# Kernel tuning notes

Measured on AMD Instinct MI355X. Metric: run time of the kernel, lower is better.

The kernel has to match this reference:

```python
import jax, jax.numpy as jnp
import numpy as np

D_MODEL = 1024
D_STATE = 16
D_CONV = 4
EXPAND = 2
D_INNER = EXPAND * D_MODEL  # 2048
DT_RANK = (D_MODEL + 15) // 16  # 64
BATCH = 2
SEQ = 1024


def setup_inputs() -> dict:
    key = jax.random.key(0)
    ks = jax.random.split(key, 9)
    s = 0.02
    x = jax.random.normal(ks[0], (BATCH, SEQ, D_MODEL), jnp.float32)
    W_in = jax.random.normal(ks[1], (D_MODEL, 2 * D_INNER), jnp.float32) * s
    conv_w = jax.random.normal(ks[2], (D_INNER, D_CONV), jnp.float32) * s
    conv_b = jnp.zeros((D_INNER,), jnp.float32)
    W_x = jax.random.normal(ks[3], (D_INNER, DT_RANK + 2 * D_STATE), jnp.float32) * s
    W_dt = jax.random.normal(ks[4], (DT_RANK, D_INNER), jnp.float32) * (DT_RANK ** -0.5)
    # dt bias init: inverse softplus of dt ~ U(1e-3, 0.1)
    dt0 = jax.random.uniform(ks[5], (D_INNER,), jnp.float32, 1e-3, 0.1)
    b_dt = dt0 + jnp.log(-jnp.expm1(-dt0))
    # S4D-real A init: A[d, n] = -(n+1)
    A_log = jnp.log(jnp.tile(jnp.arange(1, D_STATE + 1, dtype=jnp.float32), (D_INNER, 1)))
    D_skip = jnp.ones((D_INNER,), jnp.float32)
    W_out = jax.random.normal(ks[6], (D_INNER, D_MODEL), jnp.float32) * s
    return {"x": x, "W_in": W_in, "conv_w": conv_w, "conv_b": conv_b,
            "W_x": W_x, "W_dt": W_dt, "b_dt": b_dt, "A_log": A_log,
            "D_skip": D_skip, "W_out": W_out}


def _mamba_forward(x, W_in, conv_w, conv_b, W_x, W_dt, b_dt, A_log, D_skip, W_out):
    Bsz, L, _ = x.shape
    # input projection -> [B, L, 2*d_inner], split into stream and gate
    xz = x @ W_in
    xr, z = jnp.split(xz, 2, axis=-1)
    # depthwise causal conv1d over time
    xt = xr.transpose(0, 2, 1)                       # [B, d_inner, L]
    kern = conv_w[:, None, :]                        # [d_inner, 1, d_conv]
    xc = jax.lax.conv_general_dilated(
        xt, kern, window_strides=(1,), padding=[(D_CONV - 1, 0)],
        feature_group_count=D_INNER, dimension_numbers=("NCH", "OIH", "NCH"))
    xc = jax.nn.silu(xc + conv_b[None, :, None]).transpose(0, 2, 1)  # [B, L, d_inner]
    # data-dependent dt, B, C
    dbl = xc @ W_x                                   # [B, L, dt_rank + 2*d_state]
    dt, Bm, Cm = jnp.split(dbl, [DT_RANK, DT_RANK + D_STATE], axis=-1)
    dt = jax.nn.softplus(dt @ W_dt + b_dt)           # [B, L, d_inner]
    A = -jnp.exp(A_log)                              # [d_inner, d_state]

    def step(h, inp):
        dt_t, B_t, C_t, x_t = inp                    # [B,d_inner],[B,d_state],[B,d_state],[B,d_inner]
        dA = jnp.exp(dt_t[..., None] * A)            # [B, d_inner, d_state]
        h = dA * h + (dt_t * x_t)[..., None] * B_t[:, None, :]
        y = jnp.einsum("bds,bs->bd", h, C_t)
        return h, y

    h0 = jnp.zeros((Bsz, D_INNER, D_STATE), x.dtype)
    xs = (dt.transpose(1, 0, 2), Bm.transpose(1, 0, 2),
          Cm.transpose(1, 0, 2), xc.transpose(1, 0, 2))
    _, ys = jax.lax.scan(step, h0, xs)               # ys: [L, B, d_inner]
    y = ys.transpose(1, 0, 2) + xc * D_skip
    y = y * jax.nn.silu(z)
    return y @ W_out                                 # [B, L, d_model]


def reference(x, W_in, conv_w, conv_b, W_x, W_dt, b_dt, A_log, D_skip, W_out):
    return _mamba_forward(x, W_in, conv_w, conv_b, W_x, W_dt, b_dt, A_log, D_skip, W_out)
```

## Files before the change

kernel.cpp:

```cpp
#include <hip/hip_runtime.h>

#define BATCH 2
#define SEQL 1024
#define DMODEL 1024
#define DINNER 2048
#define DSTATE 16
#define DTRANK 64
#define NCH 64
#define LC 16

typedef short bf16x8 __attribute__((ext_vector_type(8)));
typedef float f32x4 __attribute__((ext_vector_type(4)));
typedef int i32x4 __attribute__((ext_vector_type(4)));

__device__ __forceinline__ unsigned short f2bf(float f) {
  unsigned u = __float_as_uint(f);
  return (unsigned short)((u + 0x7fffu + ((u >> 16) & 1u)) >> 16);
}
__device__ __forceinline__ float bf2f(unsigned short u) {
  return __uint_as_float((unsigned)u << 16);
}
__device__ __forceinline__ float sigmoidf_(float x) { return 1.f / (1.f + __expf(-x)); }

__device__ __forceinline__ void gl_lds16(const unsigned short* g, unsigned short* l) {
  __builtin_amdgcn_global_load_lds(
      (const __attribute__((address_space(1))) unsigned int*)g,
      (__attribute__((address_space(3))) unsigned int*)l, 16, 0, 0);
}

#define BM 128
#define BN 128

__global__ __launch_bounds__(256) void k_gemm_mfma(
    const unsigned short* __restrict__ A,
    const unsigned short* __restrict__ Bt,
    float* __restrict__ C, unsigned short* __restrict__ C2,
    int M, int N, int K, const float* __restrict__ bias, int mode)
{
  __shared__ __attribute__((aligned(16))) unsigned short As[128 * 64];
  __shared__ __attribute__((aligned(16))) unsigned short Bs[128 * 64];
  const int tid = threadIdx.x;
  const int wave = tid >> 6, lane = tid & 63;
  const int gx = gridDim.x;
  const int nwg = gx * gridDim.y;
  const int flat = blockIdx.x + gx * blockIdx.y;
  const int sw = (flat & 7) * (nwg >> 3) + (flat >> 3);
  const int m0 = (sw % gx) * BM, n0 = (sw / gx) * BN;
  const int Kc = K / gridDim.z;
  const int k0beg = blockIdx.z * Kc;
  float* Cz = C + (size_t)blockIdx.z * M * N;
  unsigned short* C2z = C2 + (size_t)blockIdx.z * M * N;
  const int wr = (wave >> 1) * 64, wc = (wave & 1) * 64;
  const int fr = lane & 15;
  const int qw = lane >> 4;

  int srow[4], scol[4];
  #pragma unroll
  for (int i = 0; i < 4; ++i) {
    int off = wave * 4096 + i * 1024 + lane * 16;
    int row = off >> 7;
    int c16 = ((off >> 4) & 7) ^ (row & 7);
    srow[i] = row;
    scol[i] = c16 * 8;
  }

  f32x4 acc[4][4] = {};
  for (int k0 = k0beg; k0 < k0beg + Kc; k0 += 64) {
    #pragma unroll
    for (int i = 0; i < 4; ++i)
      gl_lds16(A + (size_t)(m0 + srow[i]) * K + k0 + scol[i],
               &As[(wave * 4096 + i * 1024) >> 1]);
    #pragma unroll
    for (int i = 0; i < 4; ++i)
      gl_lds16(Bt + (size_t)(n0 + srow[i]) * K + k0 + scol[i],
               &Bs[(wave * 4096 + i * 1024) >> 1]);
    __syncthreads();
    #pragma unroll
    for (int t = 0; t < 2; ++t) {
      bf16x8 af[4], bfv[4];
      #pragma unroll
      for (int i = 0; i < 4; ++i) {
        int row = wr + i * 16 + fr;
        int c16 = (t * 4 + qw) ^ (row & 7);
        af[i] = *(const bf16x8*)&As[row * 64 + c16 * 8];
      }
      #pragma unroll
      for (int j = 0; j < 4; ++j) {
        int row = wc + j * 16 + fr;
        int c16 = (t * 4 + qw) ^ (row & 7);
        bfv[j] = *(const bf16x8*)&Bs[row * 64 + c16 * 8];
      }
      #pragma unroll
      for (int i = 0; i < 4; ++i)
        #pragma unroll
        for (int j = 0; j < 4; ++j)
          acc[i][j] = __builtin_amdgcn_mfma_f32_16x16x32_bf16(af[i], bfv[j], acc[i][j], 0, 0, 0);
    }
    __syncthreads();
  }
  const int rr = qw * 4;
  if (mode == 1) {
    #pragma unroll
    for (int j = 0; j < 4; ++j) {
      float bj = bias[n0 + wc + j * 16 + fr];
      #pragma unroll
      for (int i = 0; i < 4; ++i)
        #pragma unroll
        for (int r = 0; r < 4; ++r) {
          float v = acc[i][j][r] + bj;
          C2[(size_t)(m0 + wr + i * 16 + rr + r) * N + (n0 + wc + j * 16 + fr)] =
              f2bf(__logf(1.f + __expf(v)));
        }
    }
  } else if (mode == 3) {
    #pragma unroll
    for (int i = 0; i < 4; ++i)
      #pragma unroll
      for (int j = 0; j < 4; ++j)
        #pragma unroll
        for (int r = 0; r < 4; ++r)
          C2z[(size_t)(m0 + wr + i * 16 + rr + r) * N + (n0 + wc + j * 16 + fr)] =
              f2bf(acc[i][j][r]);
  } else {
    #pragma unroll
    for (int i = 0; i < 4; ++i)
      #pragma unroll
      for (int j = 0; j < 4; ++j)
        #pragma unroll
        for (int r = 0; r < 4; ++r)
          Cz[(size_t)(m0 + wr + i * 16 + rr + r) * N + (n0 + wc + j * 16 + fr)] = acc[i][j][r];
  }
}

__global__ __launch_bounds__(256) void k_gemm_n64(
    const unsigned short* __restrict__ A,
    const unsigned short* __restrict__ Bt,
    unsigned short* __restrict__ C2, int M, int N, int K)
{
  __shared__ __attribute__((aligned(16))) unsigned short As[128 * 64];
  __shared__ __attribute__((aligned(16))) unsigned short Bs[64 * 64];
  const int tid = threadIdx.x;
  const int wave = tid >> 6, lane = tid & 63;
  const int gx = gridDim.x;
  const int nwg = gx * gridDim.y;
  const int flat = blockIdx.x + gx * blockIdx.y;
  const int sw = (flat & 7) * (nwg >> 3) + (flat >> 3);
  const int m0 = (sw % gx) * 128, n0 = (sw / gx) * 64;
  const int wr = (wave & 1) * 64, wc = (wave >> 1) * 32;
  const int fr = lane & 15;
  const int qw = lane >> 4;

  int srowA[4], scolA[4];
  #pragma unroll
  for (int i = 0; i < 4; ++i) {
    int off = wave * 4096 + i * 1024 + lane * 16;
    int row = off >> 7;
    int c16 = ((off >> 4) & 7) ^ (row & 7);
    srowA[i] = row;
    scolA[i] = c16 * 8;
  }
  int srowB[2], scolB[2];
  #pragma unroll
  for (int i = 0; i < 2; ++i) {
    int off = wave * 2048 + i * 1024 + lane * 16;
    int row = off >> 7;
    int c16 = ((off >> 4) & 7) ^ (row & 7);
    srowB[i] = row;
    scolB[i] = c16 * 8;
  }

  f32x4 acc[4][2] = {};
  for (int k0 = 0; k0 < K; k0 += 64) {
    #pragma unroll
    for (int i = 0; i < 4; ++i)
      gl_lds16(A + (size_t)(m0 + srowA[i]) * K + k0 + scolA[i],
               &As[(wave * 4096 + i * 1024) >> 1]);
    #pragma unroll
    for (int i = 0; i < 2; ++i)
      gl_lds16(Bt + (size_t)(n0 + srowB[i]) * K + k0 + scolB[i],
               &Bs[(wave * 2048 + i * 1024) >> 1]);
    __syncthreads();
    #pragma unroll
    for (int t = 0; t < 2; ++t) {
      bf16x8 af[4], bfv[2];
      #pragma unroll
      for (int i = 0; i < 4; ++i) {
        int row = wr + i * 16 + fr;
        int c16 = (t * 4 + qw) ^ (row & 7);
        af[i] = *(const bf16x8*)&As[row * 64 + c16 * 8];
      }
      #pragma unroll
      for (int j = 0; j < 2; ++j) {
        int row = wc + j * 16 + fr;
        int c16 = (t * 4 + qw) ^ (row & 7);
        bfv[j] = *(const bf16x8*)&Bs[row * 64 + c16 * 8];
      }
      #pragma unroll
      for (int i = 0; i < 4; ++i)
        #pragma unroll
        for (int j = 0; j < 2; ++j)
          acc[i][j] = __builtin_amdgcn_mfma_f32_16x16x32_bf16(af[i], bfv[j], acc[i][j], 0, 0, 0);
    }
    __syncthreads();
  }
  const int rr = qw * 4;
  #pragma unroll
  for (int i = 0; i < 4; ++i)
    #pragma unroll
    for (int j = 0; j < 2; ++j)
      #pragma unroll
      for (int r = 0; r < 4; ++r)
        C2[(size_t)(m0 + wr + i * 16 + rr + r) * N + (n0 + wc + j * 16 + fr)] =
            f2bf(acc[i][j][r]);
}

__device__ __forceinline__ void transpose_tile(
    const float* __restrict__ src, unsigned short* __restrict__ dst,
    int R, int C, int bx, int by, float* t )
{
  int bc = bx * 64, br = by * 64;
  int tr = threadIdx.x >> 2;
  int tc = (threadIdx.x & 3) * 16;
  #pragma unroll
  for (int i = 0; i < 4; ++i) {
    float4 v = *(const float4*)(src + (size_t)(br + tr) * C + bc + tc + i * 4);
    t[tr * 65 + tc + i * 4 + 0] = v.x; t[tr * 65 + tc + i * 4 + 1] = v.y;
    t[tr * 65 + tc + i * 4 + 2] = v.z; t[tr * 65 + tc + i * 4 + 3] = v.w;
  }
  __syncthreads();
  unsigned short tmp[16];
  #pragma unroll
  for (int i = 0; i < 16; ++i) tmp[i] = f2bf(t[(tc + i) * 65 + tr]);
  unsigned short* dp = dst + (size_t)(bc + tr) * R + br + tc;
  *(i32x4*)dp = *(i32x4*)&tmp[0];
  *(i32x4*)(dp + 8) = *(i32x4*)&tmp[8];
}

__global__ __launch_bounds__(256) void k_prep(
    const float* __restrict__ x,   unsigned short* __restrict__ xbf,
    const float* __restrict__ Win, unsigned short* __restrict__ wint,
    const float* __restrict__ Wout,unsigned short* __restrict__ woutt,
    const float* __restrict__ Wdt, unsigned short* __restrict__ wdtt,
    const float* __restrict__ Wx,  unsigned short* __restrict__ wxt)
{
  __shared__ float t[64 * 65];
  int bid = blockIdx.x;
  if (bid < 1024) {
    int i = (bid * 256 + threadIdx.x) * 8;
    float4 a = *(const float4*)(x + i);
    float4 b = *(const float4*)(x + i + 4);
    unsigned short tmp[8] = {f2bf(a.x), f2bf(a.y), f2bf(a.z), f2bf(a.w),
                             f2bf(b.x), f2bf(b.y), f2bf(b.z), f2bf(b.w)};
    *(i32x4*)(xbf + i) = *(i32x4*)tmp;
  } else if (bid < 2048) {
    int tt = bid - 1024;
    transpose_tile(Win, wint, 1024, 4096, tt & 63, tt >> 6, t);
  } else if (bid < 2560) {
    int tt = bid - 2048;
    transpose_tile(Wout, woutt, 2048, 1024, tt & 15, tt >> 4, t);
  } else if (bid < 2592) {
    int tt = bid - 2560;
    transpose_tile(Wdt, wdtt, 64, 2048, tt, 0, t);
  } else {
    int idx = (bid - 2592) * 256 + threadIdx.x;
    int k = idx & (DINNER - 1);
    int n = idx >> 11;
    float v = (n < 96) ? Wx[(size_t)k * 96 + n] : 0.f;
    wxt[idx] = f2bf(v);
  }
}

__global__ __launch_bounds__(256) void k_conv_silu(
    const unsigned short* __restrict__ xzb, const float* __restrict__ cw,
    const float* __restrict__ cb, unsigned short* __restrict__ xcb)
{
  int t = blockIdx.x * 256 + threadIdx.x;
  int idx = t * 8;
  int d0 = idx & (DINNER - 1);
  int bl = idx >> 11;
  int l = bl & (SEQL - 1);
  float s[8];
  {
    float4 c0 = *(const float4*)(cb + d0);
    float4 c1 = *(const float4*)(cb + d0 + 4);
    s[0] = c0.x; s[1] = c0.y; s[2] = c0.z; s[3] = c0.w;
    s[4] = c1.x; s[5] = c1.y; s[6] = c1.z; s[7] = c1.w;
  }
  float4 w[8];
  #pragma unroll
  for (int i = 0; i < 8; ++i) w[i] = *(const float4*)(cw + (d0 + i) * 4);
  #pragma unroll
  for (int k = 0; k < 4; ++k) {
    int ll = l - 3 + k;
    if (ll >= 0) {
      bf16x8 v = *(const bf16x8*)&xzb[(size_t)(bl - 3 + k) * 4096 + d0];
      #pragma unroll
      for (int i = 0; i < 8; ++i)
        s[i] += bf2f((unsigned short)v[i]) * ((const float*)&w[i])[k];
    }
  }
  unsigned short o[8];
  #pragma unroll
  for (int i = 0; i < 8; ++i) {
    float r = s[i] * sigmoidf_(s[i]);
    o[i] = f2bf(r);
  }
  *(i32x4*)&xcb[idx] = *(i32x4*)o;
}

__global__ void k_reduce2(const float* __restrict__ part, float* __restrict__ dbl,
                          unsigned short* __restrict__ dtraw)
{
  int idx = blockIdx.x * 256 + threadIdx.x;
  float s = 0.f;
  #pragma unroll
  for (int z = 0; z < 16; ++z) s += part[(size_t)z * 2048 * 128 + idx];
  dbl[idx] = s;
  int col = idx & 127, rw = idx >> 7;
  if (col < 64) dtraw[rw * 64 + col] = f2bf(s);
}

__global__ void k_reduce5(const unsigned short* __restrict__ part, float* __restrict__ out)
{
  int idx = (blockIdx.x * 256 + threadIdx.x) * 8;
  float s[8] = {};
  #pragma unroll
  for (int z = 0; z < 4; ++z) {
    bf16x8 v = *(const bf16x8*)(part + (size_t)z * 2048 * 1024 + idx);
    #pragma unroll
    for (int i = 0; i < 8; ++i) s[i] += bf2f((unsigned short)v[i]);
  }
  *(f32x4*)(out + idx) = *(f32x4*)&s[0];
  *(f32x4*)(out + idx + 4) = *(f32x4*)&s[4];
}

__global__ __launch_bounds__(256) void k_scan_A(
    const unsigned short* __restrict__ dtb, const unsigned short* __restrict__ xcb,
    const float* __restrict__ dbl, const float* __restrict__ Alog,
    float* __restrict__ hend, float* __restrict__ sumdtb)
{
  __shared__ __attribute__((aligned(16))) float bcB[LC][DSTATE];
  int gid = blockIdx.x * 256 + threadIdx.x;
  int d = gid & (DINNER - 1);
  int t = gid >> 11;
  int c = t & (NCH - 1);
  int b = t >> 6;
  const int r0 = b * SEQL + c * LC;
  bcB[threadIdx.x >> 4][threadIdx.x & 15] =
      dbl[(size_t)(r0 + (threadIdx.x >> 4)) * 128 + 64 + (threadIdx.x & 15)];
  float As[DSTATE];
  #pragma unroll
  for (int i = 0; i < 4; ++i) {
    f32x4 a = *(const f32x4*)&Alog[d * DSTATE + i * 4];
    #pragma unroll
    for (int j = 0; j < 4; ++j) As[i * 4 + j] = -__expf(a[j]);
  }
  __syncthreads();
  float h[DSTATE];
  #pragma unroll
  for (int s = 0; s < DSTATE; ++s) h[s] = 0.f;
  float sumdt = 0.f;
  #pragma unroll
  for (int li = 0; li < LC; li += 2) {
    float dt0 = bf2f(dtb[(size_t)(r0 + li) * DINNER + d]);
    float xv0 = bf2f(xcb[(size_t)(r0 + li) * DINNER + d]);
    float dt1 = bf2f(dtb[(size_t)(r0 + li + 1) * DINNER + d]);
    float xv1 = bf2f(xcb[(size_t)(r0 + li + 1) * DINNER + d]);
    f32x4 B0[4], B1[4];
    #pragma unroll
    for (int i = 0; i < 4; ++i) B0[i] = *(const f32x4*)&bcB[li][i * 4];
    #pragma unroll
    for (int i = 0; i < 4; ++i) B1[i] = *(const f32x4*)&bcB[li + 1][i * 4];
    float dtx0 = dt0 * xv0, dtx1 = dt1 * xv1;
    sumdt += dt0 + dt1;
    const float* Bv0 = (const float*)B0;
    const float* Bv1 = (const float*)B1;
    #pragma unroll
    for (int s = 0; s < DSTATE; ++s) {
      float dA0 = __expf(dt0 * As[s]);
      h[s] = dA0 * h[s] + dtx0 * Bv0[s];
      float dA1 = __expf(dt1 * As[s]);
      h[s] = dA1 * h[s] + dtx1 * Bv1[s];
    }
  }
  size_t base = ((size_t)(b * NCH + c) * DSTATE) * DINNER + d;
  #pragma unroll
  for (int s = 0; s < DSTATE; ++s) hend[base + (size_t)s * DINNER] = h[s];
  sumdtb[(size_t)(b * NCH + c) * DINNER + d] = sumdt;
}

__global__ void k_scan_B(const float* __restrict__ hend, const float* __restrict__ sumdtb,
                         const float* __restrict__ Alog, float* __restrict__ hin)
{
  int gid = blockIdx.x * 256 + threadIdx.x;
  int d = gid & (DINNER - 1);
  int s = (gid >> 11) & (DSTATE - 1);
  int b = gid >> 15;
  const float As = -__expf(Alog[d * DSTATE + s]);
  float h = 0.f;
  for (int c0 = 0; c0 < NCH; c0 += 8) {
    float he[8], sd[8];
    #pragma unroll
    for (int i = 0; i < 8; ++i) {
      he[i] = hend[((size_t)(b * NCH + c0 + i) * DSTATE + s) * DINNER + d];
      sd[i] = sumdtb[(size_t)(b * NCH + c0 + i) * DINNER + d];
    }
    #pragma unroll
    for (int i = 0; i < 8; ++i) {
      hin[((size_t)(b * NCH + c0 + i) * DSTATE + s) * DINNER + d] = h;
      h = __expf(sd[i] * As) * h + he[i];
    }
  }
}

__global__ __launch_bounds__(256) void k_scan_C(
    const unsigned short* __restrict__ dtb, const unsigned short* __restrict__ xcb,
    const float* __restrict__ dbl, const float* __restrict__ Alog,
    const float* __restrict__ hin, const float* __restrict__ Dskip,
    const unsigned short* __restrict__ xzb, unsigned short* __restrict__ yact)
{
  __shared__ __attribute__((aligned(16))) float bc[LC][32];
  int gid = blockIdx.x * 256 + threadIdx.x;
  int d = gid & (DINNER - 1);
  int t = gid >> 11;
  int c = t & (NCH - 1);
  int b = t >> 6;
  const int r0 = b * SEQL + c * LC;
  {
    int step = threadIdx.x >> 4, j = (threadIdx.x & 15) * 2;
    float2 v = *(const float2*)&dbl[(size_t)(r0 + step) * 128 + 64 + j];
    bc[step][j] = v.x; bc[step][j + 1] = v.y;
  }
  float As[DSTATE];
  #pragma unroll
  for (int i = 0; i < 4; ++i) {
    f32x4 a = *(const f32x4*)&Alog[d * DSTATE + i * 4];
    #pragma unroll
    for (int j = 0; j < 4; ++j) As[i * 4 + j] = -__expf(a[j]);
  }
  float h[DSTATE];
  size_t base = ((size_t)(b * NCH + c) * DSTATE) * DINNER + d;
  #pragma unroll
  for (int s = 0; s < DSTATE; ++s) h[s] = hin[base + (size_t)s * DINNER];
  const float dsk = Dskip[d];
  __syncthreads();
  #pragma unroll
  for (int li = 0; li < LC; li += 2) {
    const int r = r0 + li;
    float dt0 = bf2f(dtb[(size_t)r * DINNER + d]);
    float xv0 = bf2f(xcb[(size_t)r * DINNER + d]);
    float zv0 = bf2f(xzb[(size_t)r * 4096 + 2048 + d]);
    float dt1 = bf2f(dtb[(size_t)(r + 1) * DINNER + d]);
    float xv1 = bf2f(xcb[(size_t)(r + 1) * DINNER + d]);
    float zv1 = bf2f(xzb[(size_t)(r + 1) * 4096 + 2048 + d]);
    f32x4 B0[4], C0[4], B1[4], C1[4];
    #pragma unroll
    for (int i = 0; i < 4; ++i) B0[i] = *(const f32x4*)&bc[li][i * 4];
    #pragma unroll
    for (int i = 0; i < 4; ++i) C0[i] = *(const f32x4*)&bc[li][16 + i * 4];
    #pragma unroll
    for (int i = 0; i < 4; ++i) B1[i] = *(const f32x4*)&bc[li + 1][i * 4];
    #pragma unroll
    for (int i = 0; i < 4; ++i) C1[i] = *(const f32x4*)&bc[li + 1][16 + i * 4];
    const float* Bv0 = (const float*)B0; const float* Cv0 = (const float*)C0;
    const float* Bv1 = (const float*)B1; const float* Cv1 = (const float*)C1;
    float dtx0 = dt0 * xv0, dtx1 = dt1 * xv1;
    float y0 = 0.f, y1 = 0.f;
    #pragma unroll
    for (int s = 0; s < DSTATE; ++s) {
      float dA0 = __expf(dt0 * As[s]);
      h[s] = dA0 * h[s] + dtx0 * Bv0[s];
      y0 += h[s] * Cv0[s];
      float dA1 = __expf(dt1 * As[s]);
      h[s] = dA1 * h[s] + dtx1 * Bv1[s];
      y1 += h[s] * Cv1[s];
    }
    y0 += xv0 * dsk;
    y1 += xv1 * dsk;
    float ya0 = y0 * (zv0 * sigmoidf_(zv0));
    float ya1 = y1 * (zv1 * sigmoidf_(zv1));
    yact[(size_t)r * DINNER + d] = f2bf(ya0);
    yact[(size_t)(r + 1) * DINNER + d] = f2bf(ya1);
  }
}

extern "C" void kernel_launch(void* const* d_in, const int* in_sizes, int n_in,
                              void* d_out, int out_size, void* d_ws, size_t ws_size,
                              hipStream_t stream) {
  const float* x     = (const float*)d_in[0];
  const float* Win   = (const float*)d_in[1];
  const float* cw    = (const float*)d_in[2];
  const float* cbias = (const float*)d_in[3];
  const float* Wx    = (const float*)d_in[4];
  const float* Wdt   = (const float*)d_in[5];
  const float* bdt   = (const float*)d_in[6];
  const float* Alog  = (const float*)d_in[7];
  const float* Dsk   = (const float*)d_in[8];
  const float* Wout  = (const float*)d_in[9];
  float* out = (float*)d_out;

  char* ws = (char*)d_ws;
  const size_t MB = 1 << 20;
  unsigned short* xzb   = (unsigned short*)(ws);
  unsigned short* xbf   = (unsigned short*)(ws + 16 * MB);
  unsigned short* wint  = (unsigned short*)(ws + 20 * MB);
  unsigned short* xcb   = (unsigned short*)(ws + 28 * MB);
  unsigned short* wxt   = (unsigned short*)(ws + 36 * MB);
  float*          dbl   = (float*)         (ws + 37 * MB);
  unsigned short* dtraw = (unsigned short*)(ws + 38 * MB);
  unsigned short* wdtt  = (unsigned short*)(ws + 39 * MB);
  unsigned short* dtb16 = (unsigned short*)(ws + 40 * MB);
  float*          hend  = (float*)         (ws + 48 * MB);
  float*          sumdt = (float*)         (ws + 64 * MB);
  float*          hin   = (float*)         (ws + 66 * MB);
  unsigned short* yact  = (unsigned short*)(ws + 82 * MB);
  unsigned short* woutt = (unsigned short*)(ws + 90 * MB);
  float*          part2 = (float*)         (ws + 94 * MB);
  unsigned short* part5 = (unsigned short*)(ws + 110 * MB);
  (void)ws_size; (void)in_sizes; (void)n_in; (void)out_size;

  k_prep<<<3616, 256, 0, stream>>>(x, xbf, Win, wint, Wout, woutt, Wdt, wdtt, Wx, wxt);
  k_gemm_n64<<<dim3(16, 64), 256, 0, stream>>>(xbf, wint, xzb, 2048, 4096, 1024);
  k_conv_silu<<<2048, 256, 0, stream>>>(xzb, cw, cbias, xcb);
  k_gemm_mfma<<<dim3(16, 1, 16), 256, 0, stream>>>(xcb, wxt, part2, nullptr, 2048, 128, 2048, nullptr, 0);
  k_reduce2<<<1024, 256, 0, stream>>>(part2, dbl, dtraw);
  k_gemm_mfma<<<dim3(16, 16, 1), 256, 0, stream>>>(dtraw, wdtt, nullptr, dtb16, 2048, 2048, 64, bdt, 1);
  k_scan_A<<<1024, 256, 0, stream>>>(dtb16, xcb, dbl, Alog, hend, sumdt);
  k_scan_B<<<256, 256, 0, stream>>>(hend, sumdt, Alog, hin);
  k_scan_C<<<1024, 256, 0, stream>>>(dtb16, xcb, dbl, Alog, hin, Dsk, xzb, yact);
  k_gemm_mfma<<<dim3(16, 8, 4), 256, 0, stream>>>(yact, woutt, nullptr, part5, 2048, 1024, 2048, nullptr, 3);
  k_reduce5<<<1024, 256, 0, stream>>>(part5, out);
}
```

Baseline: 137.5 us.

## Store scan chunk states in bf16 and route small GEMMs through n64 split-K kernel

The inter-chunk scan state buffers (hend, hin) are now stored as bf16 instead of fp32, which halves their traffic between the three scan kernels. The n64 GEMM kernel gains split-K and an output-mode parameter. It now handles the x_proj GEMM (split-K of 8 instead of 16) and the out-projection (split-K of 2 instead of 4), and the reduction kernels are adjusted to match. The bf16 state storage loses precision in the carried recurrent state.

```diff
diff --git a/kernel.cpp b/kernel.cpp
--- a/kernel.cpp
+++ b/kernel.cpp
@@ -135,7 +135,8 @@
 __global__ __launch_bounds__(256) void k_gemm_n64(
     const unsigned short* __restrict__ A,
     const unsigned short* __restrict__ Bt,
-    unsigned short* __restrict__ C2, int M, int N, int K)
+    float* __restrict__ C, unsigned short* __restrict__ C2,
+    int M, int N, int K, int mode)
 {
   __shared__ __attribute__((aligned(16))) unsigned short As[128 * 64];
   __shared__ __attribute__((aligned(16))) unsigned short Bs[64 * 64];
@@ -146,6 +147,10 @@
   const int flat = blockIdx.x + gx * blockIdx.y;
   const int sw = (flat & 7) * (nwg >> 3) + (flat >> 3);
   const int m0 = (sw % gx) * 128, n0 = (sw / gx) * 64;
+  const int Kc = K / gridDim.z;
+  const int k0beg = blockIdx.z * Kc;
+  float* Cz = C + (size_t)blockIdx.z * M * N;
+  unsigned short* C2z = C2 + (size_t)blockIdx.z * M * N;
   const int wr = (wave & 1) * 64, wc = (wave >> 1) * 32;
   const int fr = lane & 15;
   const int qw = lane >> 4;
@@ -170,7 +175,7 @@
   }
 
   f32x4 acc[4][2] = {};
-  for (int k0 = 0; k0 < K; k0 += 64) {
+  for (int k0 = k0beg; k0 < k0beg + Kc; k0 += 64) {
     #pragma unroll
     for (int i = 0; i < 4; ++i)
       gl_lds16(A + (size_t)(m0 + srowA[i]) * K + k0 + scolA[i],
@@ -204,14 +209,34 @@
     __syncthreads();
   }
   const int rr = qw * 4;
-  #pragma unroll
-  for (int i = 0; i < 4; ++i)
-    #pragma unroll
-    for (int j = 0; j < 2; ++j)
-      #pragma unroll
-      for (int r = 0; r < 4; ++r)
-        C2[(size_t)(m0 + wr + i * 16 + rr + r) * N + (n0 + wc + j * 16 + fr)] =
-            f2bf(acc[i][j][r]);
+  if (mode == 2) {
+    #pragma unroll
+    for (int i = 0; i < 4; ++i)
+      #pragma unroll
+      for (int j = 0; j < 2; ++j)
+        #pragma unroll
+        for (int r = 0; r < 4; ++r)
+          C2[(size_t)(m0 + wr + i * 16 + rr + r) * N + (n0 + wc + j * 16 + fr)] =
+              f2bf(acc[i][j][r]);
+  } else if (mode == 3) {
+    #pragma unroll
+    for (int i = 0; i < 4; ++i)
+      #pragma unroll
+      for (int j = 0; j < 2; ++j)
+        #pragma unroll
+        for (int r = 0; r < 4; ++r)
+          C2z[(size_t)(m0 + wr + i * 16 + rr + r) * N + (n0 + wc + j * 16 + fr)] =
+              f2bf(acc[i][j][r]);
+  } else {
+    #pragma unroll
+    for (int i = 0; i < 4; ++i)
+      #pragma unroll
+      for (int j = 0; j < 2; ++j)
+        #pragma unroll
+        for (int r = 0; r < 4; ++r)
+          Cz[(size_t)(m0 + wr + i * 16 + rr + r) * N + (n0 + wc + j * 16 + fr)] =
+              acc[i][j][r];
+  }
 }
 
 __device__ __forceinline__ void transpose_tile(
@@ -314,7 +339,7 @@
   int idx = blockIdx.x * 256 + threadIdx.x;
   float s = 0.f;
   #pragma unroll
-  for (int z = 0; z < 16; ++z) s += part[(size_t)z * 2048 * 128 + idx];
+  for (int z = 0; z < 8; ++z) s += part[(size_t)z * 2048 * 128 + idx];
   dbl[idx] = s;
   int col = idx & 127, rw = idx >> 7;
   if (col < 64) dtraw[rw * 64 + col] = f2bf(s);
@@ -325,7 +350,7 @@
   int idx = (blockIdx.x * 256 + threadIdx.x) * 8;
   float s[8] = {};
   #pragma unroll
-  for (int z = 0; z < 4; ++z) {
+  for (int z = 0; z < 2; ++z) {
     bf16x8 v = *(const bf16x8*)(part + (size_t)z * 2048 * 1024 + idx);
     #pragma unroll
     for (int i = 0; i < 8; ++i) s[i] += bf2f((unsigned short)v[i]);
@@ -337,7 +362,7 @@
 __global__ __launch_bounds__(256) void k_scan_A(
     const unsigned short* __restrict__ dtb, const unsigned short* __restrict__ xcb,
     const float* __restrict__ dbl, const float* __restrict__ Alog,
-    float* __restrict__ hend, float* __restrict__ sumdtb)
+    unsigned short* __restrict__ hendb, float* __restrict__ sumdtb)
 {
   __shared__ __attribute__((aligned(16))) float bcB[LC][DSTATE];
   int gid = blockIdx.x * 256 + threadIdx.x;
@@ -385,12 +410,14 @@
   }
   size_t base = ((size_t)(b * NCH + c) * DSTATE) * DINNER + d;
   #pragma unroll
-  for (int s = 0; s < DSTATE; ++s) hend[base + (size_t)s * DINNER] = h[s];
+  for (int s = 0; s < DSTATE; ++s) hendb[base + (size_t)s * DINNER] = f2bf(h[s]);
   sumdtb[(size_t)(b * NCH + c) * DINNER + d] = sumdt;
 }
 
-__global__ void k_scan_B(const float* __restrict__ hend, const float* __restrict__ sumdtb,
-                         const float* __restrict__ Alog, float* __restrict__ hin)
+__global__ void k_scan_B(const unsigned short* __restrict__ hendb,
+                         const float* __restrict__ sumdtb,
+                         const float* __restrict__ Alog,
+                         unsigned short* __restrict__ hinb)
 {
   int gid = blockIdx.x * 256 + threadIdx.x;
   int d = gid & (DINNER - 1);
@@ -402,12 +429,12 @@
     float he[8], sd[8];
     #pragma unroll
     for (int i = 0; i < 8; ++i) {
-      he[i] = hend[((size_t)(b * NCH + c0 + i) * DSTATE + s) * DINNER + d];
+      he[i] = bf2f(hendb[((size_t)(b * NCH + c0 + i) * DSTATE + s) * DINNER + d]);
       sd[i] = sumdtb[(size_t)(b * NCH + c0 + i) * DINNER + d];
     }
     #pragma unroll
     for (int i = 0; i < 8; ++i) {
-      hin[((size_t)(b * NCH + c0 + i) * DSTATE + s) * DINNER + d] = h;
+      hinb[((size_t)(b * NCH + c0 + i) * DSTATE + s) * DINNER + d] = f2bf(h);
       h = __expf(sd[i] * As) * h + he[i];
     }
   }
@@ -416,7 +443,7 @@
 __global__ __launch_bounds__(256) void k_scan_C(
     const unsigned short* __restrict__ dtb, const unsigned short* __restrict__ xcb,
     const float* __restrict__ dbl, const float* __restrict__ Alog,
-    const float* __restrict__ hin, const float* __restrict__ Dskip,
+    const unsigned short* __restrict__ hinb, const float* __restrict__ Dskip,
     const unsigned short* __restrict__ xzb, unsigned short* __restrict__ yact)
 {
   __shared__ __attribute__((aligned(16))) float bc[LC][32];
@@ -441,7 +468,7 @@
   float h[DSTATE];
   size_t base = ((size_t)(b * NCH + c) * DSTATE) * DINNER + d;
   #pragma unroll
-  for (int s = 0; s < DSTATE; ++s) h[s] = hin[base + (size_t)s * DINNER];
+  for (int s = 0; s < DSTATE; ++s) h[s] = bf2f(hinb[base + (size_t)s * DINNER]);
   const float dsk = Dskip[d];
   __syncthreads();
   #pragma unroll
@@ -510,24 +537,24 @@
   unsigned short* dtraw = (unsigned short*)(ws + 38 * MB);
   unsigned short* wdtt  = (unsigned short*)(ws + 39 * MB);
   unsigned short* dtb16 = (unsigned short*)(ws + 40 * MB);
-  float*          hend  = (float*)         (ws + 48 * MB);
-  float*          sumdt = (float*)         (ws + 64 * MB);
-  float*          hin   = (float*)         (ws + 66 * MB);
-  unsigned short* yact  = (unsigned short*)(ws + 82 * MB);
-  unsigned short* woutt = (unsigned short*)(ws + 90 * MB);
-  float*          part2 = (float*)         (ws + 94 * MB);
-  unsigned short* part5 = (unsigned short*)(ws + 110 * MB);
+  unsigned short* hendb = (unsigned short*)(ws + 48 * MB);
+  float*          sumdt = (float*)         (ws + 56 * MB);
+  unsigned short* hinb  = (unsigned short*)(ws + 57 * MB);
+  unsigned short* yact  = (unsigned short*)(ws + 65 * MB);
+  unsigned short* woutt = (unsigned short*)(ws + 73 * MB);
+  float*          part2 = (float*)         (ws + 77 * MB);
+  unsigned short* part5 = (unsigned short*)(ws + 85 * MB);
   (void)ws_size; (void)in_sizes; (void)n_in; (void)out_size;
 
   k_prep<<<3616, 256, 0, stream>>>(x, xbf, Win, wint, Wout, woutt, Wdt, wdtt, Wx, wxt);
-  k_gemm_n64<<<dim3(16, 64), 256, 0, stream>>>(xbf, wint, xzb, 2048, 4096, 1024);
+  k_gemm_n64<<<dim3(16, 64, 1), 256, 0, stream>>>(xbf, wint, nullptr, xzb, 2048, 4096, 1024, 2);
   k_conv_silu<<<2048, 256, 0, stream>>>(xzb, cw, cbias, xcb);
-  k_gemm_mfma<<<dim3(16, 1, 16), 256, 0, stream>>>(xcb, wxt, part2, nullptr, 2048, 128, 2048, nullptr, 0);
+  k_gemm_n64<<<dim3(16, 2, 8), 256, 0, stream>>>(xcb, wxt, part2, nullptr, 2048, 128, 2048, 0);
   k_reduce2<<<1024, 256, 0, stream>>>(part2, dbl, dtraw);
   k_gemm_mfma<<<dim3(16, 16, 1), 256, 0, stream>>>(dtraw, wdtt, nullptr, dtb16, 2048, 2048, 64, bdt, 1);
-  k_scan_A<<<1024, 256, 0, stream>>>(dtb16, xcb, dbl, Alog, hend, sumdt);
-  k_scan_B<<<256, 256, 0, stream>>>(hend, sumdt, Alog, hin);
-  k_scan_C<<<1024, 256, 0, stream>>>(dtb16, xcb, dbl, Alog, hin, Dsk, xzb, yact);
-  k_gemm_mfma<<<dim3(16, 8, 4), 256, 0, stream>>>(yact, woutt, nullptr, part5, 2048, 1024, 2048, nullptr, 3);
+  k_scan_A<<<1024, 256, 0, stream>>>(dtb16, xcb, dbl, Alog, hendb, sumdt);
+  k_scan_B<<<256, 256, 0, stream>>>(hendb, sumdt, Alog, hinb);
+  k_scan_C<<<1024, 256, 0, stream>>>(dtb16, xcb, dbl, Alog, hinb, Dsk, xzb, yact);
+  k_gemm_n64<<<dim3(16, 16, 2), 256, 0, stream>>>(yact, woutt, nullptr, part5, 2048, 1024, 2048, 3);
   k_reduce5<<<1024, 256, 0, stream>>>(part5, out);
 }
```

Result: no change. 136.9 us (-0.4%).
